# Kernel optimization log

Hardware: AMD Instinct MI355X
Metric: run time of the kernel (lower is better)

Reference implementation:

```python
import jax, jax.numpy as jnp
import numpy as np

D = 512
H = 8
DH = D // H
EPS = 1e-5


def _layernorm(x, g, b):
    mu = jnp.mean(x, axis=-1, keepdims=True)
    var = jnp.mean((x - mu) ** 2, axis=-1, keepdims=True)
    return (x - mu) * jax.lax.rsqrt(var + EPS) * g + b


def setup_inputs() -> dict:
    key = jax.random.key(0)
    ks = jax.random.split(key, 10)
    B, S = 4, 2048
    s = 1.0 / np.sqrt(D)
    return {
        "x": jax.random.normal(ks[0], (B, S, D), dtype=jnp.float32),
        "Wq": jax.random.normal(ks[1], (D, D), dtype=jnp.float32) * s,
        "Wk": jax.random.normal(ks[2], (D, D), dtype=jnp.float32) * s,
        "Wv": jax.random.normal(ks[3], (D, D), dtype=jnp.float32) * s,
        "Wo": jax.random.normal(ks[4], (D, D), dtype=jnp.float32) * s,
        "W1": jax.random.normal(ks[5], (4 * D, D), dtype=jnp.float32) * s,
        "b1": jnp.zeros((4 * D,), dtype=jnp.float32),
        "W2": jax.random.normal(ks[6], (D, 4 * D), dtype=jnp.float32) * (1.0 / np.sqrt(4 * D)),
        "b2": jnp.zeros((D,), dtype=jnp.float32),
        "g1": jnp.ones((D,), dtype=jnp.float32),
        "bb1": jnp.zeros((D,), dtype=jnp.float32),
        "g2": jnp.ones((D,), dtype=jnp.float32),
        "bb2": jnp.zeros((D,), dtype=jnp.float32),
    }


def reference(x, Wq, Wk, Wv, Wo, W1, b1, W2, b2, g1, bb1, g2, bb2):
    B, S, _ = x.shape
    # projections (torch Linear: y = x @ W.T), split heads: chunk(-1) == reshape to [B,S,H,DH]
    q = (x @ Wq.T).reshape(B, S, H, DH).transpose(0, 2, 1, 3)  # [B,H,S,DH]
    k = (x @ Wk.T).reshape(B, S, H, DH).transpose(0, 2, 1, 3)
    v = (x @ Wv.T).reshape(B, S, H, DH).transpose(0, 2, 1, 3)
    scores = jnp.einsum("bhsd,bhtd->bhst", q, k) / np.sqrt(DH)  # [B,H,S,S]
    attn = jax.nn.softmax(scores, axis=-1)
    ctx = jnp.einsum("bhst,bhtd->bhsd", attn, v)  # [B,H,S,DH]
    ctx = ctx.transpose(0, 2, 1, 3).reshape(B, S, D)
    h = _layernorm(x + ctx @ Wo.T, g1, bb1)
    mlp = jax.nn.relu(h @ W1.T + b1) @ W2.T + b2
    return _layernorm(h + mlp, g2, bb2)
```

## Files before the change

### kernel.cpp

```cpp
#include <hip/hip_runtime.h>
#include <hip/hip_bf16.h>
#include <cstdint>
#include <cstddef>

typedef short bf16x8 __attribute__((ext_vector_type(8)));
typedef float floatx4 __attribute__((ext_vector_type(4)));
typedef unsigned int uintx4 __attribute__((ext_vector_type(4)));
typedef unsigned short u16;

constexpr int B = 4, S = 2048, D = 512, H = 8, DH = 64;
constexpr int M_ROWS = B * S;
constexpr int D4 = 4 * D;
constexpr float QSCALE = 0.18033688011112042f;

__device__ __forceinline__ u16 f2b(float f) {
  unsigned u = __builtin_bit_cast(unsigned, f);
  u += 0x7fff + ((u >> 16) & 1);
  return (u16)(u >> 16);
}

__device__ __forceinline__ float b2f(u16 h) {
  return __builtin_bit_cast(float, (unsigned)h << 16);
}

__device__ __forceinline__ bf16x8 ldfrag(const u16* p) {
  return *reinterpret_cast<const bf16x8*>(p);
}

__device__ __forceinline__ floatx4 mfma16(bf16x8 a, bf16x8 b, floatx4 c) {
  return __builtin_amdgcn_mfma_f32_16x16x32_bf16(a, b, c, 0, 0, 0);
}

__device__ __forceinline__ ushort4 f2b4(float4 v) {
  ushort4 r;
  r.x = f2b(v.x); r.y = f2b(v.y); r.z = f2b(v.z); r.w = f2b(v.w);
  return r;
}

__device__ __forceinline__ void gld16(const u16* g, u16* l) {
  __builtin_amdgcn_global_load_lds(
      (const __attribute__((address_space(1))) void*)g,
      (__attribute__((address_space(3))) void*)l, 16, 0, 0);
}

__device__ __forceinline__ void add8bf(const u16* p, float* v) {
  const ushort4 h0 = *(const ushort4*)p, h1 = *(const ushort4*)(p + 4);
  v[0] += b2f(h0.x); v[1] += b2f(h0.y); v[2] += b2f(h0.z); v[3] += b2f(h0.w);
  v[4] += b2f(h1.x); v[5] += b2f(h1.y); v[6] += b2f(h1.z); v[7] += b2f(h1.w);
}

__global__ void cast_all_kernel(const float4* __restrict__ x,
                                const float4* __restrict__ w1, const float4* __restrict__ w2,
                                const float4* __restrict__ wq, const float4* __restrict__ wk,
                                const float4* __restrict__ wv, const float4* __restrict__ wo,
                                ushort4* __restrict__ xb,
                                ushort4* __restrict__ w1b, ushort4* __restrict__ w2b,
                                ushort4* __restrict__ wqb, ushort4* __restrict__ wkb,
                                ushort4* __restrict__ wvb, ushort4* __restrict__ wob) {
  int i = blockIdx.x * blockDim.x + threadIdx.x;
  constexpr int NX = (M_ROWS * D) / 4;
  constexpr int N1 = (D4 * D) / 4;
  constexpr int NS = (D * D) / 4;
  if (i < NX) { xb[i] = f2b4(x[i]); return; }
  i -= NX;
  if (i < N1) { w1b[i] = f2b4(w1[i]); return; }
  i -= N1;
  if (i < N1) { w2b[i] = f2b4(w2[i]); return; }
  i -= N1;
  const int sel = i >> 16, off = i & (NS - 1);
  const float4* src = sel == 0 ? wq : sel == 1 ? wk : sel == 2 ? wv : wo;
  ushort4* dst = sel == 0 ? wqb : sel == 1 ? wkb : sel == 2 ? wvb : wob;
  dst[off] = f2b4(src[off]);
}

template <int EPI, int PIPE, int NX, int NZ>
__global__ __launch_bounds__(256) void gemm_bt(
    const u16* __restrict__ A, const u16* __restrict__ W,
    const float* __restrict__ bias, void* __restrict__ out0, void* __restrict__ out1,
    int M, int N, int K, int klen) {
  __shared__ __align__(16) u16 As[PIPE ? 3 : 2][128 * 32];
  __shared__ __align__(16) u16 Bs[PIPE ? 3 : 2][128 * 32];
  const int wave = threadIdx.x >> 6, lane = threadIdx.x & 63;
  const int quad = lane >> 4, l16 = lane & 15;

  constexpr int NWG = NX * 64 * NZ;
  int wg = blockIdx.x;
  wg = (wg & 7) * (NWG / 8) + (wg >> 3);
  const int xcol = wg % NX;
  const int zz = (wg / NX) % NZ;
  const int yrow = wg / (NX * NZ);

  const int rowB = yrow * 128, colB = xcol * 128;
  const int rowW = (wave >> 1) * 64, colW = (wave & 1) * 64;
  const int koff = zz * klen;
  void* out = zz ? out1 : out0;

  floatx4 acc[4][4];
#pragma unroll
  for (int i = 0; i < 4; i++)
#pragma unroll
    for (int j = 0; j < 4; j++) acc[i][j] = (floatx4){0.f,0.f,0.f,0.f};

  const u16* gA = A + (size_t)(rowB + wave * 32 + (lane >> 2)) * K + koff + (lane & 3) * 8;
  const u16* gB = W + (size_t)(colB + wave * 32 + (lane >> 2)) * K + koff + (lane & 3) * 8;
  const int lds_off = wave * 1024;

  if constexpr (PIPE) {
    const int nt = klen / 32;
#pragma unroll
    for (int T = 0; T < 2; T++) {
      gld16(gA + T * 32,                    &As[T][lds_off]);
      gld16(gA + (size_t)16 * K + T * 32,   &As[T][lds_off + 512]);
      gld16(gB + T * 32,                    &Bs[T][lds_off]);
      gld16(gB + (size_t)16 * K + T * 32,   &Bs[T][lds_off + 512]);
    }
    int rb = 0, wb = 2;
    for (int it = 0; it < nt; ++it) {
      if (it + 1 < nt) asm volatile("s_waitcnt vmcnt(4)" ::: "memory");
      else             asm volatile("s_waitcnt vmcnt(0)" ::: "memory");
      __builtin_amdgcn_s_barrier();
      __builtin_amdgcn_sched_barrier(0);

      if (it + 2 < nt) {
        const int kc2 = (it + 2) * 32;
        gld16(gA + kc2,                    &As[wb][lds_off]);
        gld16(gA + (size_t)16 * K + kc2,   &As[wb][lds_off + 512]);
        gld16(gB + kc2,                    &Bs[wb][lds_off]);
        gld16(gB + (size_t)16 * K + kc2,   &Bs[wb][lds_off + 512]);
      }

      bf16x8 a[4], b[4];
#pragma unroll
      for (int i = 0; i < 4; i++)
        a[i] = ldfrag(&As[rb][(rowW + i * 16 + l16) * 32 + quad * 8]);
#pragma unroll
      for (int j = 0; j < 4; j++)
        b[j] = ldfrag(&Bs[rb][(colW + j * 16 + l16) * 32 + quad * 8]);
#pragma unroll
      for (int i = 0; i < 4; i++)
#pragma unroll
        for (int j = 0; j < 4; j++) acc[i][j] = mfma16(a[i], b[j], acc[i][j]);

      rb = rb == 2 ? 0 : rb + 1;
      wb = wb == 2 ? 0 : wb + 1;
    }
  } else {
#pragma unroll
    for (int rr = 0; rr < 2; rr++) {
      gld16(gA + (size_t)rr * 16 * K, &As[0][lds_off + rr * 512]);
      gld16(gB + (size_t)rr * 16 * K, &Bs[0][lds_off + rr * 512]);
    }

    int buf = 0;
    for (int kc = 0; kc < klen; kc += 32, buf ^= 1) {
      __syncthreads();

      if (kc + 32 < klen) {
#pragma unroll
        for (int rr = 0; rr < 2; rr++) {
          gld16(gA + (size_t)rr * 16 * K + kc + 32, &As[buf ^ 1][lds_off + rr * 512]);
          gld16(gB + (size_t)rr * 16 * K + kc + 32, &Bs[buf ^ 1][lds_off + rr * 512]);
        }
      }

      bf16x8 a[4], b[4];
#pragma unroll
      for (int i = 0; i < 4; i++)
        a[i] = ldfrag(&As[buf][(rowW + i * 16 + l16) * 32 + quad * 8]);
#pragma unroll
      for (int j = 0; j < 4; j++)
        b[j] = ldfrag(&Bs[buf][(colW + j * 16 + l16) * 32 + quad * 8]);
#pragma unroll
      for (int i = 0; i < 4; i++)
#pragma unroll
        for (int j = 0; j < 4; j++) acc[i][j] = mfma16(a[i], b[j], acc[i][j]);
    }
  }

#pragma unroll
  for (int i = 0; i < 4; i++) {
#pragma unroll
    for (int j = 0; j < 4; j++) {
      const int gn = colB + colW + j * 16 + l16;
      const float bv = (EPI == 1) ? bias[gn] : 0.f;
#pragma unroll
      for (int r = 0; r < 4; r++) {
        const int gm = rowB + rowW + i * 16 + quad * 4 + r;
        float v = acc[i][j][r] + bv;
        if (EPI == 1) v = v > 0.f ? v : 0.f;
        ((u16*)out)[(size_t)gm * N + gn] = f2b(v);
      }
    }
  }
}

__global__ __launch_bounds__(256) void qkv_gemm(
    const u16* __restrict__ xb,
    const u16* __restrict__ wq, const u16* __restrict__ wk, const u16* __restrict__ wv,
    u16* __restrict__ q, u16* __restrict__ k, u16* __restrict__ vT) {
  __shared__ __align__(16) u16 As[3][128 * 32];
  __shared__ __align__(16) u16 Bs[3][128 * 32];
  const int wave = threadIdx.x >> 6, lane = threadIdx.x & 63;
  const int quad = lane >> 4, l16 = lane & 15;

  int wg = blockIdx.x;
  wg = (wg & 7) * 96 + (wg >> 3);
  const int yrow = wg / 12;
  const int r12 = wg % 12;
  const int which = r12 >> 2;
  const int xcol = r12 & 3;

  const u16* __restrict__ W = which == 0 ? wq : (which == 1 ? wk : wv);
  const int rowB = yrow * 128, colB = xcol * 128;
  const int rowW = (wave >> 1) * 64, colW = (wave & 1) * 64;

  floatx4 acc[4][4];
#pragma unroll
  for (int i = 0; i < 4; i++)
#pragma unroll
    for (int j = 0; j < 4; j++) acc[i][j] = (floatx4){0.f,0.f,0.f,0.f};

  const u16* gA = xb + (size_t)(rowB + wave * 32 + (lane >> 2)) * D + (lane & 3) * 8;
  const u16* gB = W + (size_t)(colB + wave * 32 + (lane >> 2)) * D + (lane & 3) * 8;
  const int lds_off = wave * 1024;

  constexpr int nt = D / 32;
#pragma unroll
  for (int T = 0; T < 2; T++) {
    gld16(gA + T * 32,                    &As[T][lds_off]);
    gld16(gA + (size_t)16 * D + T * 32,   &As[T][lds_off + 512]);
    gld16(gB + T * 32,                    &Bs[T][lds_off]);
    gld16(gB + (size_t)16 * D + T * 32,   &Bs[T][lds_off + 512]);
  }
  int rb = 0, wb = 2;
  for (int it = 0; it < nt; ++it) {
    if (it + 1 < nt) asm volatile("s_waitcnt vmcnt(4)" ::: "memory");
    else             asm volatile("s_waitcnt vmcnt(0)" ::: "memory");
    __builtin_amdgcn_s_barrier();
    __builtin_amdgcn_sched_barrier(0);

    if (it + 2 < nt) {
      const int kc2 = (it + 2) * 32;
      gld16(gA + kc2,                    &As[wb][lds_off]);
      gld16(gA + (size_t)16 * D + kc2,   &As[wb][lds_off + 512]);
      gld16(gB + kc2,                    &Bs[wb][lds_off]);
      gld16(gB + (size_t)16 * D + kc2,   &Bs[wb][lds_off + 512]);
    }

    bf16x8 a[4], b[4];
#pragma unroll
    for (int i = 0; i < 4; i++)
      a[i] = ldfrag(&As[rb][(rowW + i * 16 + l16) * 32 + quad * 8]);
#pragma unroll
    for (int j = 0; j < 4; j++)
      b[j] = ldfrag(&Bs[rb][(colW + j * 16 + l16) * 32 + quad * 8]);
#pragma unroll
    for (int i = 0; i < 4; i++)
#pragma unroll
      for (int j = 0; j < 4; j++) acc[i][j] = mfma16(a[i], b[j], acc[i][j]);

    rb = rb == 2 ? 0 : rb + 1;
    wb = wb == 2 ? 0 : wb + 1;
  }

  const float oscale = (which == 0) ? QSCALE : 1.0f;
  u16* dst01 = which == 0 ? q : k;
#pragma unroll
  for (int i = 0; i < 4; i++) {
#pragma unroll
    for (int j = 0; j < 4; j++) {
      const int gn = colB + colW + j * 16 + l16;
      const int h = gn >> 6, dh = gn & 63;
#pragma unroll
      for (int r = 0; r < 4; r++) {
        const int gm = rowB + rowW + i * 16 + quad * 4 + r;
        const int bb = gm >> 11, s = gm & 2047;
        const u16 val = f2b(acc[i][j][r] * oscale);
        if (which < 2) {
          dst01[((((size_t)bb * H + h) * S) + s) * DH + dh] = val;
        } else {
          const int sl = s & 63;
          const int sw = (s & ~63) | (sl & 35) | ((sl & 12) << 1) | ((sl & 16) >> 2);
          vT[((((size_t)bb * H + h) * DH) + dh) * S + sw] = val;
        }
      }
    }
  }
}

__global__ __launch_bounds__(512, 4) void attn_kernel(
    const u16* __restrict__ q, const u16* __restrict__ k,
    const u16* __restrict__ vT, u16* __restrict__ ctxb) {
  __shared__ __align__(16) u16 kvbuf[4][2][4096];
  __shared__ __align__(16) float ltb[2][4][32];
  const int wave = threadIdx.x >> 6, lane = threadIdx.x & 63;
  const int quad = lane >> 4, l16 = lane & 15;
  const int pair = wave >> 1, khalf = wave & 1;
  const int blk = (blockIdx.x & 7) * 64 + (blockIdx.x >> 3);
  const int w = blk * 4 + pair;
  const int bh = w >> 6, qt = w & 63;
  const int bb = bh >> 3, h = bh & 7;

  const u16* qp = q + ((size_t)bh * S + qt * 32 + l16) * DH + quad * 8;
  bf16x8 qf[2][2];
#pragma unroll
  for (int t = 0; t < 2; t++) {
    qf[t][0] = ldfrag(qp + (size_t)t * 16 * DH);
    qf[t][1] = ldfrag(qp + (size_t)t * 16 * DH + 32);
  }

  const int ch = pair & 1;
  const int soct = ((lane & 3) ^ ((lane >> 3) & 3)) * 8;
  const u16 *g0, *g1;
  size_t gstride;
  int d0;
  if (pair < 2) {
    g0 = k + (size_t)bh * S * DH + (size_t)(khalf * 1024 + (lane >> 2)) * DH
           + ch * 32 + soct;
    g1 = g0 + (size_t)16 * DH;
    gstride = (size_t)32 * DH;
    d0 = ch * 1024;
  } else {
    g0 = vT + (size_t)bh * DH * S + (size_t)(ch * 32 + (lane >> 2)) * S
            + khalf * 1024 + soct;
    g1 = g0 + (size_t)16 * S;
    gstride = 32;
    d0 = 2048 + ch * 1024;
  }

  floatx4 o[2][4];
#pragma unroll
  for (int t = 0; t < 2; t++)
#pragma unroll
    for (int c = 0; c < 4; c++) o[t][c] = (floatx4){0.f,0.f,0.f,0.f};
  float lacc[2] = {0.f, 0.f};

  gld16(g0,           &kvbuf[0][khalf][d0]);
  gld16(g1,           &kvbuf[0][khalf][d0 + 512]);
  gld16(g0 + gstride, &kvbuf[1][khalf][d0]);
  gld16(g1 + gstride, &kvbuf[1][khalf][d0 + 512]);

  const int sq = (quad ^ ((l16 >> 1) & 3)) * 8;

  for (int it2 = 0; it2 < 16; ++it2) {
    asm volatile("s_waitcnt vmcnt(0)" ::: "memory");
    __builtin_amdgcn_s_barrier();
    __builtin_amdgcn_sched_barrier(0);
    const int b0 = (it2 & 1) * 2;

    if (it2 + 1 < 16) {
      const size_t t2 = (size_t)(2 * it2 + 2);
      gld16(g0 + t2 * gstride,       &kvbuf[b0 ^ 2][khalf][d0]);
      gld16(g1 + t2 * gstride,       &kvbuf[b0 ^ 2][khalf][d0 + 512]);
      gld16(g0 + (t2 + 1) * gstride, &kvbuf[(b0 ^ 2) + 1][khalf][d0]);
      gld16(g1 + (t2 + 1) * gstride, &kvbuf[(b0 ^ 2) + 1][khalf][d0 + 512]);
    }

#pragma unroll
    for (int half = 0; half < 2; ++half) {
      const u16* Kb = &kvbuf[b0 + half][khalf][0];
      const u16* Vb = &kvbuf[b0 + half][khalf][2048];
      bf16x8 kf[4], vf[4];
      kf[0] = ldfrag(&Kb[l16 * 32 + sq]);
      kf[1] = ldfrag(&Kb[1024 + l16 * 32 + sq]);
      kf[2] = ldfrag(&Kb[(16 + l16) * 32 + sq]);
      kf[3] = ldfrag(&Kb[1024 + (16 + l16) * 32 + sq]);
#pragma unroll
      for (int c = 0; c < 4; c++)
        vf[c] = ldfrag(&Vb[(c * 16 + l16) * 32 + sq]);

#pragma unroll
      for (int t = 0; t < 2; t++) {
        floatx4 sc[2];
#pragma unroll
        for (int i = 0; i < 2; i++) {
          floatx4 z = (floatx4){0.f,0.f,0.f,0.f};
          z = mfma16(kf[2 * i], qf[t][0], z);
          z = mfma16(kf[2 * i + 1], qf[t][1], z);
          sc[i] = z;
        }

        unsigned wd[4];
        float a = 0.f;
#pragma unroll
        for (int i = 0; i < 2; i++) {
          const float p0 = __builtin_amdgcn_exp2f(sc[i][0]);
          const float p1 = __builtin_amdgcn_exp2f(sc[i][1]);
          const float p2 = __builtin_amdgcn_exp2f(sc[i][2]);
          const float p3 = __builtin_amdgcn_exp2f(sc[i][3]);
          a += (p0 + p1) + (p2 + p3);
          wd[2 * i] = __builtin_amdgcn_perm(
              __builtin_bit_cast(unsigned, p1) + 0x8000u,
              __builtin_bit_cast(unsigned, p0) + 0x8000u, 0x07060302u);
          wd[2 * i + 1] = __builtin_amdgcn_perm(
              __builtin_bit_cast(unsigned, p3) + 0x8000u,
              __builtin_bit_cast(unsigned, p2) + 0x8000u, 0x07060302u);
        }
        lacc[t] += a;
        const uintx4 lo4 = (uintx4){wd[0], wd[1], wd[2], wd[3]};
        const bf16x8 pa = __builtin_bit_cast(bf16x8, lo4);

#pragma unroll
        for (int c = 0; c < 4; c++)
          o[t][c] = mfma16(pa, vf[c], o[t][c]);
      }
    }
  }

  float lt[2];
#pragma unroll
  for (int t = 0; t < 2; t++) {
    float l = lacc[t];
    l += __shfl_xor(l, 16);
    l += __shfl_xor(l, 32);
    lt[t] = l;
  }

  __syncthreads();
  float* ob = reinterpret_cast<float*>(&kvbuf[0][0][0]) + pair * 2048;
  if (quad == 0) {
#pragma unroll
    for (int t = 0; t < 2; t++) ltb[khalf][pair][t * 16 + l16] = lt[t];
  }
  if (khalf == 1) {
#pragma unroll
    for (int t = 0; t < 2; t++)
#pragma unroll
      for (int c = 0; c < 4; c++) {
        const int idx = 4 * t + c;
        const int slot = (idx ^ (lane & 7)) & 7;
        *reinterpret_cast<floatx4*>(&ob[lane * 32 + slot * 4]) = o[t][c];
      }
  }
  __syncthreads();
  if (khalf == 0) {
    float inv[2][4];
#pragma unroll
    for (int t = 0; t < 2; t++)
#pragma unroll
      for (int r = 0; r < 4; r++)
        inv[t][r] = 1.0f / (ltb[0][pair][t * 16 + quad * 4 + r] +
                            ltb[1][pair][t * 16 + quad * 4 + r]);

    const size_t crow_base = ((size_t)bb * S) * D + h * DH;
#pragma unroll
    for (int t = 0; t < 2; t++)
#pragma unroll
      for (int c = 0; c < 4; c++) {
        const int idx = 4 * t + c;
        const int slot = (idx ^ (lane & 7)) & 7;
        const floatx4 oo = o[t][c] +
            *reinterpret_cast<const floatx4*>(&ob[lane * 32 + slot * 4]);
        const int dh = c * 16 + l16;
#pragma unroll
        for (int r = 0; r < 4; r++) {
          const int s = qt * 32 + t * 16 + quad * 4 + r;
          ctxb[crow_base + (size_t)s * D + dh] = f2b(oo[r] * inv[t][r]);
        }
      }
  }
}

template <int MODE>
__global__ __launch_bounds__(256) void ln_kernel(
    const void* __restrict__ resid, const u16* __restrict__ ya,
    const u16* __restrict__ yb, const float* __restrict__ pb,
    const float* __restrict__ g, const float* __restrict__ bvec,
    float* __restrict__ outF, u16* __restrict__ outB) {
  const int wave = threadIdx.x >> 6, lane = threadIdx.x & 63;
  const int row = blockIdx.x * 4 + wave;
  float v[8] = {0.f, 0.f, 0.f, 0.f, 0.f, 0.f, 0.f, 0.f};
  add8bf(ya + (size_t)row * D + lane * 8, v);
  add8bf(yb + (size_t)row * D + lane * 8, v);
  add8bf((const u16*)resid + (size_t)row * D + lane * 8, v);
  if (MODE == 1) {
    const float4 p0 = *(const float4*)(pb + lane * 8);
    const float4 p1 = *(const float4*)(pb + lane * 8 + 4);
    v[0] += p0.x; v[1] += p0.y; v[2] += p0.z; v[3] += p0.w;
    v[4] += p1.x; v[5] += p1.y; v[6] += p1.z; v[7] += p1.w;
  }
  float sum = 0.f;
#pragma unroll
  for (int i = 0; i < 8; i++) sum += v[i];
#pragma unroll
  for (int d = 1; d < 64; d <<= 1) sum += __shfl_xor(sum, d);
  const float mu = sum * (1.f / D);
  float vs = 0.f;
#pragma unroll
  for (int i = 0; i < 8; i++) { const float t = v[i] - mu; vs += t * t; }
#pragma unroll
  for (int d = 1; d < 64; d <<= 1) vs += __shfl_xor(vs, d);
  const float rstd = rsqrtf(vs * (1.f / D) + 1e-5f);
#pragma unroll
  for (int i = 0; i < 8; i++) {
    const int col = lane * 8 + i;
    const float o = (v[i] - mu) * rstd * g[col] + bvec[col];
    if (MODE == 0) outB[(size_t)row * D + col] = f2b(o);
    else           outF[(size_t)row * D + col] = o;
  }
}

constexpr size_t OFF_XB  = 0;
constexpr size_t OFF_WQB = 8u << 20;
constexpr size_t OFF_WKB = OFF_WQB + (512u << 10);
constexpr size_t OFF_WVB = OFF_WKB + (512u << 10);
constexpr size_t OFF_WOB = OFF_WVB + (512u << 10);
constexpr size_t OFF_W1B = 10u << 20;
constexpr size_t OFF_W2B = 12u << 20;
constexpr size_t OFF_Q   = 14u << 20;
constexpr size_t OFF_K   = 22u << 20;
constexpr size_t OFF_VT  = 30u << 20;
constexpr size_t OFF_CTX = 38u << 20;
constexpr size_t OFF_Y   = 46u << 20;
constexpr size_t OFF_HB  = 78u << 20;
constexpr size_t OFF_M1B = 86u << 20;

extern "C" void kernel_launch(void* const* d_in, const int* in_sizes, int n_in,
                              void* d_out, int out_size, void* d_ws, size_t ws_size,
                              hipStream_t stream) {
  const float* x  = (const float*)d_in[0];
  const float* Wq = (const float*)d_in[1];
  const float* Wk = (const float*)d_in[2];
  const float* Wv = (const float*)d_in[3];
  const float* Wo = (const float*)d_in[4];
  const float* W1 = (const float*)d_in[5];
  const float* b1 = (const float*)d_in[6];
  const float* W2 = (const float*)d_in[7];
  const float* b2 = (const float*)d_in[8];
  const float* g1 = (const float*)d_in[9];
  const float* bb1 = (const float*)d_in[10];
  const float* g2 = (const float*)d_in[11];
  const float* bb2 = (const float*)d_in[12];

  char* ws = (char*)d_ws;
  u16* xb  = (u16*)(ws + OFF_XB);
  u16* wqb = (u16*)(ws + OFF_WQB);
  u16* wkb = (u16*)(ws + OFF_WKB);
  u16* wvb = (u16*)(ws + OFF_WVB);
  u16* wob = (u16*)(ws + OFF_WOB);
  u16* w1b = (u16*)(ws + OFF_W1B);
  u16* w2b = (u16*)(ws + OFF_W2B);
  u16* qb  = (u16*)(ws + OFF_Q);
  u16* kb  = (u16*)(ws + OFF_K);
  u16* vtb = (u16*)(ws + OFF_VT);
  u16* ctxb = (u16*)(ws + OFF_CTX);
  u16* y0 = (u16*)(ws + OFF_Y);
  u16* y1 = (u16*)(ws + OFF_Q);
  u16* hb  = (u16*)(ws + OFF_HB);
  u16* m1b = (u16*)(ws + OFF_M1B);

  {
    const int n4 = (M_ROWS * D) / 4 + (D4 * D) / 4 * 2 + (D * D) / 4 * 4;
    cast_all_kernel<<<(n4 + 255) / 256, 256, 0, stream>>>(
        (const float4*)x, (const float4*)W1, (const float4*)W2, (const float4*)Wq,
        (const float4*)Wk, (const float4*)Wv, (const float4*)Wo,
        (ushort4*)xb, (ushort4*)w1b, (ushort4*)w2b, (ushort4*)wqb,
        (ushort4*)wkb, (ushort4*)wvb, (ushort4*)wob);
  }

  qkv_gemm<<<768, 256, 0, stream>>>(xb, wqb, wkb, wvb, qb, kb, vtb);

  attn_kernel<<<B * H * S / 32 / 4, 512, 0, stream>>>(qb, kb, vtb, ctxb);

  gemm_bt<0, 1, 4, 2><<<512, 256, 0, stream>>>(
      ctxb, wob, nullptr, y0, y1, M_ROWS, D, D, D / 2);

  ln_kernel<0><<<M_ROWS / 4, 256, 0, stream>>>(
      xb, y0, y1, nullptr, g1, bb1, nullptr, hb);

  gemm_bt<1, 0, 16, 1><<<1024, 256, 0, stream>>>(
      hb, w1b, b1, m1b, nullptr, M_ROWS, D4, D, D);

  gemm_bt<0, 1, 4, 2><<<512, 256, 0, stream>>>(
      m1b, w2b, nullptr, y0, y1, M_ROWS, D, D4, D4 / 2);

  ln_kernel<1><<<M_ROWS / 4, 256, 0, stream>>>(
      hb, y0, y1, b2, g2, bb2, (float*)d_out, nullptr);
}
```

Baseline: 246.9 us.

## Switch GEMM kernels to 32x32x16 MFMA with XOR-swizzled LDS layout

Replaces the 16x16x32 bf16 MFMA tiling in the generic GEMM and the QKV GEMM with 32x32x16 MFMA. Each wave now computes 2x2 32x32 blocks with fewer LDS fragment loads per MFMA. LDS chunks are XOR-swizzled at load time and un-swizzled on read, to cut bank conflicts when 32 lanes read consecutive rows. The epilogue indexing changes to match the 32x32 accumulator layout, which brings a risk of layout bugs and less favourable store coalescing.

```diff
diff --git a/kernel.cpp b/kernel.cpp
--- a/kernel.cpp
+++ b/kernel.cpp
@@ -5,6 +5,7 @@
 
 typedef short bf16x8 __attribute__((ext_vector_type(8)));
 typedef float floatx4 __attribute__((ext_vector_type(4)));
+typedef float floatx16 __attribute__((ext_vector_type(16)));
 typedef unsigned int uintx4 __attribute__((ext_vector_type(4)));
 typedef unsigned short u16;
 
@@ -29,6 +30,10 @@
 
 __device__ __forceinline__ floatx4 mfma16(bf16x8 a, bf16x8 b, floatx4 c) {
   return __builtin_amdgcn_mfma_f32_16x16x32_bf16(a, b, c, 0, 0, 0);
+}
+
+__device__ __forceinline__ floatx16 mfma32(bf16x8 a, bf16x8 b, floatx16 c) {
+  return __builtin_amdgcn_mfma_f32_32x32x16_bf16(a, b, c, 0, 0, 0);
 }
 
 __device__ __forceinline__ ushort4 f2b4(float4 v) {
@@ -81,7 +86,7 @@
   __shared__ __align__(16) u16 As[PIPE ? 3 : 2][128 * 32];
   __shared__ __align__(16) u16 Bs[PIPE ? 3 : 2][128 * 32];
   const int wave = threadIdx.x >> 6, lane = threadIdx.x & 63;
-  const int quad = lane >> 4, l16 = lane & 15;
+  const int l32 = lane & 31, hi = lane >> 5, g2 = (lane >> 1) & 3;
 
   constexpr int NWG = NX * 64 * NZ;
   int wg = blockIdx.x;
@@ -95,14 +100,17 @@
   const int koff = zz * klen;
   void* out = zz ? out1 : out0;
 
-  floatx4 acc[4][4];
-#pragma unroll
-  for (int i = 0; i < 4; i++)
-#pragma unroll
-    for (int j = 0; j < 4; j++) acc[i][j] = (floatx4){0.f,0.f,0.f,0.f};
-
-  const u16* gA = A + (size_t)(rowB + wave * 32 + (lane >> 2)) * K + koff + (lane & 3) * 8;
-  const u16* gB = W + (size_t)(colB + wave * 32 + (lane >> 2)) * K + koff + (lane & 3) * 8;
+  floatx16 acc[2][2];
+#pragma unroll
+  for (int i = 0; i < 2; i++)
+#pragma unroll
+    for (int j = 0; j < 2; j++)
+#pragma unroll
+      for (int r = 0; r < 16; r++) acc[i][j][r] = 0.f;
+
+  const int soct = ((lane & 3) ^ ((lane >> 3) & 3)) * 8;
+  const u16* gA = A + (size_t)(rowB + wave * 32 + (lane >> 2)) * K + koff + soct;
+  const u16* gB = W + (size_t)(colB + wave * 32 + (lane >> 2)) * K + koff + soct;
   const int lds_off = wave * 1024;
 
   if constexpr (PIPE) {
@@ -129,17 +137,22 @@
         gld16(gB + (size_t)16 * K + kc2,   &Bs[wb][lds_off + 512]);
       }
 
-      bf16x8 a[4], b[4];
-#pragma unroll
-      for (int i = 0; i < 4; i++)
-        a[i] = ldfrag(&As[rb][(rowW + i * 16 + l16) * 32 + quad * 8]);
-#pragma unroll
-      for (int j = 0; j < 4; j++)
-        b[j] = ldfrag(&Bs[rb][(colW + j * 16 + l16) * 32 + quad * 8]);
-#pragma unroll
-      for (int i = 0; i < 4; i++)
-#pragma unroll
-        for (int j = 0; j < 4; j++) acc[i][j] = mfma16(a[i], b[j], acc[i][j]);
+      bf16x8 a[2][2], b[2][2];
+#pragma unroll
+      for (int ri = 0; ri < 2; ri++)
+#pragma unroll
+        for (int ks = 0; ks < 2; ks++) {
+          const int sl = ((ks * 2 + hi) ^ g2) * 8;
+          a[ri][ks] = ldfrag(&As[rb][(rowW + ri * 32 + l32) * 32 + sl]);
+          b[ri][ks] = ldfrag(&Bs[rb][(colW + ri * 32 + l32) * 32 + sl]);
+        }
+#pragma unroll
+      for (int ri = 0; ri < 2; ri++)
+#pragma unroll
+        for (int cj = 0; cj < 2; cj++)
+#pragma unroll
+          for (int ks = 0; ks < 2; ks++)
+            acc[ri][cj] = mfma32(a[ri][ks], b[cj][ks], acc[ri][cj]);
 
       rb = rb == 2 ? 0 : rb + 1;
       wb = wb == 2 ? 0 : wb + 1;
@@ -163,30 +176,35 @@
         }
       }
 
-      bf16x8 a[4], b[4];
-#pragma unroll
-      for (int i = 0; i < 4; i++)
-        a[i] = ldfrag(&As[buf][(rowW + i * 16 + l16) * 32 + quad * 8]);
-#pragma unroll
-      for (int j = 0; j < 4; j++)
-        b[j] = ldfrag(&Bs[buf][(colW + j * 16 + l16) * 32 + quad * 8]);
-#pragma unroll
-      for (int i = 0; i < 4; i++)
-#pragma unroll
-        for (int j = 0; j < 4; j++) acc[i][j] = mfma16(a[i], b[j], acc[i][j]);
-    }
-  }
-
-#pragma unroll
-  for (int i = 0; i < 4; i++) {
-#pragma unroll
-    for (int j = 0; j < 4; j++) {
-      const int gn = colB + colW + j * 16 + l16;
+      bf16x8 a[2][2], b[2][2];
+#pragma unroll
+      for (int ri = 0; ri < 2; ri++)
+#pragma unroll
+        for (int ks = 0; ks < 2; ks++) {
+          const int sl = ((ks * 2 + hi) ^ g2) * 8;
+          a[ri][ks] = ldfrag(&As[buf][(rowW + ri * 32 + l32) * 32 + sl]);
+          b[ri][ks] = ldfrag(&Bs[buf][(colW + ri * 32 + l32) * 32 + sl]);
+        }
+#pragma unroll
+      for (int ri = 0; ri < 2; ri++)
+#pragma unroll
+        for (int cj = 0; cj < 2; cj++)
+#pragma unroll
+          for (int ks = 0; ks < 2; ks++)
+            acc[ri][cj] = mfma32(a[ri][ks], b[cj][ks], acc[ri][cj]);
+    }
+  }
+
+#pragma unroll
+  for (int ri = 0; ri < 2; ri++) {
+#pragma unroll
+    for (int cj = 0; cj < 2; cj++) {
+      const int gn = colB + colW + cj * 32 + l32;
       const float bv = (EPI == 1) ? bias[gn] : 0.f;
 #pragma unroll
-      for (int r = 0; r < 4; r++) {
-        const int gm = rowB + rowW + i * 16 + quad * 4 + r;
-        float v = acc[i][j][r] + bv;
+      for (int reg = 0; reg < 16; reg++) {
+        const int gm = rowB + rowW + ri * 32 + (reg & 3) + 8 * (reg >> 2) + 4 * hi;
+        float v = acc[ri][cj][reg] + bv;
         if (EPI == 1) v = v > 0.f ? v : 0.f;
         ((u16*)out)[(size_t)gm * N + gn] = f2b(v);
       }
@@ -201,7 +219,7 @@
   __shared__ __align__(16) u16 As[3][128 * 32];
   __shared__ __align__(16) u16 Bs[3][128 * 32];
   const int wave = threadIdx.x >> 6, lane = threadIdx.x & 63;
-  const int quad = lane >> 4, l16 = lane & 15;
+  const int l32 = lane & 31, hi = lane >> 5, g2 = (lane >> 1) & 3;
 
   int wg = blockIdx.x;
   wg = (wg & 7) * 96 + (wg >> 3);
@@ -214,14 +232,17 @@
   const int rowB = yrow * 128, colB = xcol * 128;
   const int rowW = (wave >> 1) * 64, colW = (wave & 1) * 64;
 
-  floatx4 acc[4][4];
-#pragma unroll
-  for (int i = 0; i < 4; i++)
-#pragma unroll
-    for (int j = 0; j < 4; j++) acc[i][j] = (floatx4){0.f,0.f,0.f,0.f};
-
-  const u16* gA = xb + (size_t)(rowB + wave * 32 + (lane >> 2)) * D + (lane & 3) * 8;
-  const u16* gB = W + (size_t)(colB + wave * 32 + (lane >> 2)) * D + (lane & 3) * 8;
+  floatx16 acc[2][2];
+#pragma unroll
+  for (int i = 0; i < 2; i++)
+#pragma unroll
+    for (int j = 0; j < 2; j++)
+#pragma unroll
+      for (int r = 0; r < 16; r++) acc[i][j][r] = 0.f;
+
+  const int soct = ((lane & 3) ^ ((lane >> 3) & 3)) * 8;
+  const u16* gA = xb + (size_t)(rowB + wave * 32 + (lane >> 2)) * D + soct;
+  const u16* gB = W + (size_t)(colB + wave * 32 + (lane >> 2)) * D + soct;
   const int lds_off = wave * 1024;
 
   constexpr int nt = D / 32;
@@ -247,17 +268,22 @@
       gld16(gB + (size_t)16 * D + kc2,   &Bs[wb][lds_off + 512]);
     }
 
-    bf16x8 a[4], b[4];
-#pragma unroll
-    for (int i = 0; i < 4; i++)
-      a[i] = ldfrag(&As[rb][(rowW + i * 16 + l16) * 32 + quad * 8]);
-#pragma unroll
-    for (int j = 0; j < 4; j++)
-      b[j] = ldfrag(&Bs[rb][(colW + j * 16 + l16) * 32 + quad * 8]);
-#pragma unroll
-    for (int i = 0; i < 4; i++)
-#pragma unroll
-      for (int j = 0; j < 4; j++) acc[i][j] = mfma16(a[i], b[j], acc[i][j]);
+    bf16x8 a[2][2], b[2][2];
+#pragma unroll
+    for (int ri = 0; ri < 2; ri++)
+#pragma unroll
+      for (int ks = 0; ks < 2; ks++) {
+        const int sl = ((ks * 2 + hi) ^ g2) * 8;
+        a[ri][ks] = ldfrag(&As[rb][(rowW + ri * 32 + l32) * 32 + sl]);
+        b[ri][ks] = ldfrag(&Bs[rb][(colW + ri * 32 + l32) * 32 + sl]);
+      }
+#pragma unroll
+    for (int ri = 0; ri < 2; ri++)
+#pragma unroll
+      for (int cj = 0; cj < 2; cj++)
+#pragma unroll
+        for (int ks = 0; ks < 2; ks++)
+          acc[ri][cj] = mfma32(a[ri][ks], b[cj][ks], acc[ri][cj]);
 
     rb = rb == 2 ? 0 : rb + 1;
     wb = wb == 2 ? 0 : wb + 1;
@@ -266,16 +292,16 @@
   const float oscale = (which == 0) ? QSCALE : 1.0f;
   u16* dst01 = which == 0 ? q : k;
 #pragma unroll
-  for (int i = 0; i < 4; i++) {
-#pragma unroll
-    for (int j = 0; j < 4; j++) {
-      const int gn = colB + colW + j * 16 + l16;
+  for (int ri = 0; ri < 2; ri++) {
+#pragma unroll
+    for (int cj = 0; cj < 2; cj++) {
+      const int gn = colB + colW + cj * 32 + l32;
       const int h = gn >> 6, dh = gn & 63;
 #pragma unroll
-      for (int r = 0; r < 4; r++) {
-        const int gm = rowB + rowW + i * 16 + quad * 4 + r;
+      for (int reg = 0; reg < 16; reg++) {
+        const int gm = rowB + rowW + ri * 32 + (reg & 3) + 8 * (reg >> 2) + 4 * hi;
         const int bb = gm >> 11, s = gm & 2047;
-        const u16 val = f2b(acc[i][j][r] * oscale);
+        const u16 val = f2b(acc[ri][cj][reg] * oscale);
         if (which < 2) {
           dst01[((((size_t)bb * H + h) * S) + s) * DH + dh] = val;
         } else {
```

Result: no change. 248.7 us (+0.8%).
